# Performance work log

Hardware: AMD Instinct MI355X
Metric: run time of the kernel (lower is better)

## Reference

```python
import jax, jax.numpy as jnp
import numpy as np

N_NODES = 100000
N_EDGES = 1600000
F_IN = 64
HIDDEN = 64
N_CLASSES = 2


def setup_inputs() -> dict:
    key = jax.random.key(0)
    k1, k2, k3, k4, k5, k6 = jax.random.split(key, 6)
    x = jax.random.normal(k1, (N_NODES, F_IN), dtype=jnp.float32)
    edge_index = jax.random.randint(k2, (2, N_EDGES), 0, N_NODES, dtype=jnp.int64)
    # Glorot-ish init for GCNConv linear weights, zero bias (PyG default)
    W1 = jax.random.normal(k3, (F_IN, HIDDEN), dtype=jnp.float32) * (1.0 / np.sqrt(F_IN))
    b1 = jnp.zeros((HIDDEN,), dtype=jnp.float32)
    W2 = jax.random.normal(k4, (HIDDEN, N_CLASSES), dtype=jnp.float32) * (1.0 / np.sqrt(HIDDEN))
    b2 = jnp.zeros((N_CLASSES,), dtype=jnp.float32)
    return {"x": x, "edge_index": edge_index, "W1": W1, "b1": b1, "W2": W2, "b2": b2}


def _gcn_norm(edge_index, num_nodes):
    # Add self-loops, then symmetric normalization D^-1/2 (A+I) D^-1/2
    loops = jnp.arange(num_nodes, dtype=edge_index.dtype)
    row = jnp.concatenate([edge_index[0], loops])  # [E+N] targets
    col = jnp.concatenate([edge_index[1], loops])  # [E+N] sources
    deg = jax.ops.segment_sum(jnp.ones(row.shape[0], jnp.float32), row, num_segments=num_nodes)
    dinv = jnp.where(deg > 0, jax.lax.rsqrt(deg), 0.0)
    norm = dinv[row] * dinv[col]  # [E+N]
    return row, col, norm


def _gcn_conv(x, W, b, row, col, norm, num_nodes):
    h = x @ W                                   # [N, out]
    msg = h[col] * norm[:, None]                # gather + scale, [E+N, out]
    agg = jax.ops.segment_sum(msg, row, num_segments=num_nodes)  # scatter-add
    return agg + b


def reference(x, edge_index, W1, b1, W2, b2):
    n = x.shape[0]
    row, col, norm = _gcn_norm(edge_index, n)
    h = jax.nn.relu(_gcn_conv(x, W1, b1, row, col, norm, n))
    # dropout p=0.5 is identity in eval mode
    logits = _gcn_conv(h, W2, b2, row, col, norm, n)
    return jax.nn.softmax(logits, axis=1)
```

## Files before the change

### kernel.cpp

```cpp
#include <hip/hip_runtime.h>
#include <hip/hip_fp16.h>


typedef _Float16 f16x8 __attribute__((ext_vector_type(8)));
typedef float f32x4 __attribute__((ext_vector_type(4)));

#define CAPSH 12
#define CAP (1 << CAPSH)
#define NBK 784

__global__ __launch_bounds__(256) void k_bin(const int* __restrict__ row,
                                             const int* __restrict__ col,
                                             int* __restrict__ relcur,
                                             unsigned* __restrict__ pairbuf,
                                             __half* __restrict__ hp,
                                             int E, int nb, int N) {
    __shared__ unsigned items[4096];
    __shared__ unsigned short bktid[4096];
    __shared__ int cnt[NBK];
    __shared__ int start0[NBK];
    __shared__ int cursor[NBK];
    __shared__ int gbase[NBK];

    int tid = threadIdx.x;
    int base = blockIdx.x * 4096;
    int m = E - base; if (m > 4096) m = 4096;

    for (int t = tid; t < nb; t += 256) cnt[t] = 0;
    __syncthreads();
    for (int i = tid; i < m; i += 256) atomicAdd(&cnt[row[base + i] >> 7], 1);
    __syncthreads();
    if (tid < 64) {
        int lane = tid, running = 0;
        for (int ch = 0; ch < 13; ++ch) {
            int idx = ch * 64 + lane;
            int v = (idx < nb) ? cnt[idx] : 0;
            int s = v;
#pragma unroll
            for (int off = 1; off < 64; off <<= 1) {
                int t = __shfl_up(s, off, 64);
                if (lane >= off) s += t;
            }
            if (idx < nb) { start0[idx] = running + s - v; cursor[idx] = running + s - v; }
            running += __shfl(s, 63, 64);
        }
    }
    __syncthreads();
    for (int i = tid; i < m; i += 256) {
        int r = row[base + i];
        int c = col[base + i];
        int b = r >> 7;
        int pos = atomicAdd(&cursor[b], 1);
        items[pos] = ((unsigned)(r & 127) << 24) | (unsigned)c;
        bktid[pos] = (unsigned short)b;
    }
    __syncthreads();
    for (int t = tid; t < nb; t += 256) {
        int cv = cnt[t];
        if (cv > 0) gbase[t] = (t << CAPSH) + atomicAdd(&relcur[t], cv);
    }
    __syncthreads();
    for (int i = tid; i < m; i += 256) {
        int b = bktid[i];
        pairbuf[gbase[b] + (i - start0[b])] = items[i];
    }
    if (blockIdx.x == 0 && tid < 32) ((int*)(hp + (size_t)N * 64))[tid] = 0;
}

__global__ __launch_bounds__(256, 4) void k_sortgemm(const unsigned* __restrict__ pairbuf,
                                                     const int* __restrict__ relcur,
                                                     const float* __restrict__ x,
                                                     const float* __restrict__ W1,
                                                     int* __restrict__ scol,
                                                     int* __restrict__ offsets,
                                                     int* __restrict__ deg,
                                                     float* __restrict__ dinv,
                                                     __half* __restrict__ hp,
                                                     int N, int nb) {
    __shared__ int cnt[256];
    __shared__ int tmp[256];
    __shared__ int cur[256];
    __shared__ float sdinv[128];
    int b = blockIdx.x;
    int tid = threadIdx.x;
    int lane = tid & 63, q = lane >> 4, mm = lane & 15;
    f16x8 bf[4][2];
#pragma unroll
    for (int nt = 0; nt < 4; ++nt)
#pragma unroll
        for (int kk = 0; kk < 2; ++kk)
#pragma unroll
            for (int j = 0; j < 8; ++j)
                bf[nt][kk][j] = (_Float16)W1[(kk * 32 + q * 8 + j) * 64 + nt * 16 + mm];

    int lo = b << CAPSH;
    int hi = lo + relcur[b];
    cnt[tid] = 0;
    __syncthreads();
    for (int i = lo + tid; i < hi; i += 256)
        atomicAdd(&cnt[pairbuf[i] >> 24], 1);
    __syncthreads();
    int cv = cnt[tid];
    tmp[tid] = cv;
    __syncthreads();
    for (int d = 1; d < 256; d <<= 1) {
        int t = (tid >= d) ? tmp[tid - d] : 0;
        __syncthreads();
        if (tid >= d) tmp[tid] += t;
        __syncthreads();
    }
    int excl = tmp[tid] - cv;
    int n0 = b << 7;
    if (tid < 128) {
        int n = n0 + tid;
        float dv = rsqrtf((float)(cv + 1));
        if (n < N) { offsets[n] = lo + excl; deg[n] = cv; dinv[n] = dv; }
        sdinv[tid] = dv;
    }
    cur[tid] = lo + excl;
    if (b == 0 && tid == 0) {
        offsets[N] = 0; deg[N] = 0;
        scol[nb << CAPSH] = N;
    }
    __syncthreads();
    for (int i = lo + tid; i < hi; i += 256) {
        unsigned it = pairbuf[i];
        int pos = atomicAdd(&cur[it >> 24], 1);
        scol[pos] = (int)(it & 0xFFFFFFu);
    }
    __syncthreads();
    int nn = N - n0; if (nn > 128) nn = 128;
    for (int t = (tid >> 6); t < (nn >> 4); t += 4) {
        const float* xrow = x + (size_t)(n0 + t * 16 + mm) * 64;
        float4 u0 = *(const float4*)(xrow + q * 8);
        float4 u1 = *(const float4*)(xrow + q * 8 + 4);
        float4 u2 = *(const float4*)(xrow + 32 + q * 8);
        float4 u3 = *(const float4*)(xrow + 32 + q * 8 + 4);
        f16x8 a0, a1;
        a0[0] = (_Float16)u0.x; a0[1] = (_Float16)u0.y; a0[2] = (_Float16)u0.z; a0[3] = (_Float16)u0.w;
        a0[4] = (_Float16)u1.x; a0[5] = (_Float16)u1.y; a0[6] = (_Float16)u1.z; a0[7] = (_Float16)u1.w;
        a1[0] = (_Float16)u2.x; a1[1] = (_Float16)u2.y; a1[2] = (_Float16)u2.z; a1[3] = (_Float16)u2.w;
        a1[4] = (_Float16)u3.x; a1[5] = (_Float16)u3.y; a1[6] = (_Float16)u3.z; a1[7] = (_Float16)u3.w;
        f32x4 ac0 = {0.f, 0.f, 0.f, 0.f}, ac1 = ac0, ac2 = ac0, ac3 = ac0;
        ac0 = __builtin_amdgcn_mfma_f32_16x16x32_f16(a0, bf[0][0], ac0, 0, 0, 0);
        ac1 = __builtin_amdgcn_mfma_f32_16x16x32_f16(a0, bf[1][0], ac1, 0, 0, 0);
        ac2 = __builtin_amdgcn_mfma_f32_16x16x32_f16(a0, bf[2][0], ac2, 0, 0, 0);
        ac3 = __builtin_amdgcn_mfma_f32_16x16x32_f16(a0, bf[3][0], ac3, 0, 0, 0);
        ac0 = __builtin_amdgcn_mfma_f32_16x16x32_f16(a1, bf[0][1], ac0, 0, 0, 0);
        ac1 = __builtin_amdgcn_mfma_f32_16x16x32_f16(a1, bf[1][1], ac1, 0, 0, 0);
        ac2 = __builtin_amdgcn_mfma_f32_16x16x32_f16(a1, bf[2][1], ac2, 0, 0, 0);
        ac3 = __builtin_amdgcn_mfma_f32_16x16x32_f16(a1, bf[3][1], ac3, 0, 0, 0);
#pragma unroll
        for (int reg = 0; reg < 4; ++reg) {
            int rl = t * 16 + q * 4 + reg;
            float dvv = sdinv[rl];
            __half* dst = hp + (size_t)(n0 + rl) * 64 + mm;
            dst[0]  = __float2half(dvv * ac0[reg]);
            dst[16] = __float2half(dvv * ac1[reg]);
            dst[32] = __float2half(dvv * ac2[reg]);
            dst[48] = __float2half(dvv * ac3[reg]);
        }
    }
}

__global__ __launch_bounds__(256, 4) void k_agg1(const __half* __restrict__ hp,
                                                 const int* __restrict__ offsets,
                                                 const int* __restrict__ deg,
                                                 const int* __restrict__ scol,
                                                 const float* __restrict__ dinv,
                                                 const float* __restrict__ b1,
                                                 const float* __restrict__ W2,
                                                 float2* __restrict__ h2p,
                                                 int N, int SENT) {
    int lane = threadIdx.x & 63;
    int slot = lane >> 3;
    int chunk = lane & 7;
    int wid = (int)((blockIdx.x * 256 + threadIdx.x) >> 6);
    int n = wid * 8 + slot;
    int nc = (n < N) ? n : N;
    int start = offsets[nc];
    int dg = deg[nc];
    int maxd = dg;
#pragma unroll
    for (int s = 8; s <= 32; s <<= 1) {
        int o = __shfl_xor(maxd, s, 64);
        maxd = (o > maxd) ? o : maxd;
    }
    const float4* hp4 = (const float4*)hp;
    float4 sr = hp4[(size_t)nc * 8 + chunk];
    __half2 acc0 = ((const __half2*)&sr)[0];
    __half2 acc1 = ((const __half2*)&sr)[1];
    __half2 acc2 = ((const __half2*)&sr)[2];
    __half2 acc3 = ((const __half2*)&sr)[3];
    for (int j0 = 0; j0 < maxd; j0 += 8) {
        int c[8];
#pragma unroll
        for (int u = 0; u < 8; ++u)
            c[u] = scol[(j0 + u < dg) ? (start + j0 + u) : SENT];
        float4 r[8];
#pragma unroll
        for (int u = 0; u < 8; ++u) r[u] = hp4[(size_t)c[u] * 8 + chunk];
#pragma unroll
        for (int u = 0; u < 8; ++u) {
            const __half2* hh = (const __half2*)&r[u];
            acc0 = __hadd2(acc0, hh[0]); acc1 = __hadd2(acc1, hh[1]);
            acc2 = __hadd2(acc2, hh[2]); acc3 = __hadd2(acc3, hh[3]);
        }
    }
    float af[8];
    { float2 f;
      f = __half22float2(acc0); af[0] = f.x; af[1] = f.y;
      f = __half22float2(acc1); af[2] = f.x; af[3] = f.y;
      f = __half22float2(acc2); af[4] = f.x; af[5] = f.y;
      f = __half22float2(acc3); af[6] = f.x; af[7] = f.y; }
    float dn = dinv[(n < N) ? n : (N - 1)];
    float4 b1a = ((const float4*)b1)[chunk * 2];
    float4 b1b = ((const float4*)b1)[chunk * 2 + 1];
    float h1[8];
    h1[0] = fmaxf(fmaf(dn, af[0], b1a.x), 0.f);
    h1[1] = fmaxf(fmaf(dn, af[1], b1a.y), 0.f);
    h1[2] = fmaxf(fmaf(dn, af[2], b1a.z), 0.f);
    h1[3] = fmaxf(fmaf(dn, af[3], b1a.w), 0.f);
    h1[4] = fmaxf(fmaf(dn, af[4], b1b.x), 0.f);
    h1[5] = fmaxf(fmaf(dn, af[5], b1b.y), 0.f);
    h1[6] = fmaxf(fmaf(dn, af[6], b1b.z), 0.f);
    h1[7] = fmaxf(fmaf(dn, af[7], b1b.w), 0.f);
    float p0 = 0.f, p1 = 0.f;
#pragma unroll
    for (int k = 0; k < 4; ++k) {
        float4 w = ((const float4*)W2)[chunk * 4 + k];
        p0 = fmaf(h1[2 * k], w.x, p0); p1 = fmaf(h1[2 * k], w.y, p1);
        p0 = fmaf(h1[2 * k + 1], w.z, p0); p1 = fmaf(h1[2 * k + 1], w.w, p1);
    }
#pragma unroll
    for (int s = 1; s <= 4; s <<= 1) {
        p0 += __shfl_xor(p0, s, 64);
        p1 += __shfl_xor(p1, s, 64);
    }
    if (chunk == 0 && n < N) h2p[n] = make_float2(dn * p0, dn * p1);
}

__global__ __launch_bounds__(256) void k_agg2(const float2* __restrict__ h2p,
                                              const int* __restrict__ offsets,
                                              const int* __restrict__ deg,
                                              const int* __restrict__ scol,
                                              const float* __restrict__ dinv,
                                              const float* __restrict__ b2,
                                              float2* __restrict__ out, int N) {
    int gtid = blockIdx.x * 256 + threadIdx.x;
    int n = gtid >> 4;
    int sub = threadIdx.x & 15;
    if (n >= N) return;
    int start = offsets[n], end = start + deg[n];
    float ax = 0.f, ay = 0.f;
    if (sub == 0) { float2 s = h2p[n]; ax = s.x; ay = s.y; }
    for (int j = start + sub; j < end; j += 16) {
        float2 v = h2p[scol[j]];
        ax += v.x; ay += v.y;
    }
#pragma unroll
    for (int s = 1; s <= 8; s <<= 1) {
        ax += __shfl_xor(ax, s, 64);
        ay += __shfl_xor(ay, s, 64);
    }
    if (sub == 0) {
        float dn = dinv[n];
        float l0 = fmaf(dn, ax, b2[0]), l1 = fmaf(dn, ay, b2[1]);
        float m = fmaxf(l0, l1);
        float e0 = __expf(l0 - m), e1 = __expf(l1 - m);
        float inv = 1.0f / (e0 + e1);
        out[n] = make_float2(e0 * inv, e1 * inv);
    }
}

extern "C" void kernel_launch(void* const* d_in, const int* in_sizes, int n_in,
                              void* d_out, int out_size, void* d_ws, size_t ws_size,
                              hipStream_t stream) {
    const float* x  = (const float*)d_in[0];
    const int*   ei = (const int*)d_in[1];
    const float* W1 = (const float*)d_in[2];
    const float* b1 = (const float*)d_in[3];
    const float* W2 = (const float*)d_in[4];
    const float* b2 = (const float*)d_in[5];
    float2* out = (float2*)d_out;

    const int N = in_sizes[0] / 64;
    const int E = in_sizes[1] / 2;
    const int nb = (N + 127) >> 7;
    const int SENT = nb << CAPSH;
    const int* row = ei;
    const int* col = ei + E;

    char* p = (char*)d_ws;
    auto alloc = [&](size_t bytes) -> void* {
        void* r = (void*)p;
        p += (bytes + 255) & ~(size_t)255;
        return r;
    };
    int*   relcur  = (int*)alloc((size_t)nb * 4);
    int*   offsets = (int*)alloc((size_t)(N + 1) * 4);
    int*   deg     = (int*)alloc((size_t)(N + 1) * 4);
    float* dinv    = (float*)alloc((size_t)N * 4);
    unsigned* pairbuf = (unsigned*)alloc((size_t)nb * CAP * 4);
    int*   scol    = (int*)alloc(((size_t)nb * CAP + 1) * 4);
    __half* hp     = (__half*)alloc((size_t)(N + 1) * 64 * 2);
    float2* h2p    = (float2*)alloc((size_t)N * 8);

    const int nTile = (E + 4095) / 4096;

    hipMemsetAsync(relcur, 0, (size_t)nb * 4, stream);
    k_bin<<<nTile, 256, 0, stream>>>(row, col, relcur, pairbuf, hp, E, nb, N);
    k_sortgemm<<<nb, 256, 0, stream>>>(pairbuf, relcur, x, W1, scol, offsets, deg, dinv, hp, N, nb);
    const int nwaves = (N + 7) / 8;
    k_agg1<<<(nwaves + 3) / 4, 256, 0, stream>>>(hp, offsets, deg, scol, dinv, b1, W2, h2p, N, SENT);
    k_agg2<<<(N * 16 + 255) / 256, 256, 0, stream>>>(h2p, offsets, deg, scol, dinv, b2, out, N);
}
```

Baseline: 166.8 us.

## Run X·W1 GEMM alongside edge binning and defer dinv scaling to sort kernel

The dense X·W1 MFMA GEMM moves out of the per-bucket sort kernel into extra blocks of the binning kernel, so it runs at the same time as edge binning. It writes an fp32 intermediate that the sort kernel later scales by dinv and converts to fp16. The Hillis-Steele shared-memory scan with many barriers is replaced by a wave-level shuffle scan over the 128 row slots. The cost is an extra fp32 round trip of N×64 values (about 25 MB of writes plus reads) and a larger workspace.

```diff
diff --git a/kernel.cpp b/kernel.cpp
--- a/kernel.cpp
+++ b/kernel.cpp
@@ -9,12 +9,15 @@
 #define CAP (1 << CAPSH)
 #define NBK 784
 
-__global__ __launch_bounds__(256) void k_bin(const int* __restrict__ row,
-                                             const int* __restrict__ col,
-                                             int* __restrict__ relcur,
-                                             unsigned* __restrict__ pairbuf,
-                                             __half* __restrict__ hp,
-                                             int E, int nb, int N) {
+__global__ __launch_bounds__(256, 4) void k_binfused(const int* __restrict__ row,
+                                                     const int* __restrict__ col,
+                                                     int* __restrict__ relcur,
+                                                     unsigned* __restrict__ pairbuf,
+                                                     __half* __restrict__ hp,
+                                                     const float* __restrict__ x,
+                                                     const float* __restrict__ W1,
+                                                     float* __restrict__ hf32,
+                                                     int E, int nb, int N, int nTileB) {
     __shared__ unsigned items[4096];
     __shared__ unsigned short bktid[4096];
     __shared__ int cnt[NBK];
@@ -23,76 +26,112 @@
     __shared__ int gbase[NBK];
 
     int tid = threadIdx.x;
-    int base = blockIdx.x * 4096;
-    int m = E - base; if (m > 4096) m = 4096;
-
-    for (int t = tid; t < nb; t += 256) cnt[t] = 0;
-    __syncthreads();
-    for (int i = tid; i < m; i += 256) atomicAdd(&cnt[row[base + i] >> 7], 1);
-    __syncthreads();
-    if (tid < 64) {
-        int lane = tid, running = 0;
-        for (int ch = 0; ch < 13; ++ch) {
-            int idx = ch * 64 + lane;
-            int v = (idx < nb) ? cnt[idx] : 0;
-            int s = v;
-#pragma unroll
-            for (int off = 1; off < 64; off <<= 1) {
-                int t = __shfl_up(s, off, 64);
-                if (lane >= off) s += t;
+
+    if (blockIdx.x < nTileB) {
+        int base = blockIdx.x * 4096;
+        int m = E - base; if (m > 4096) m = 4096;
+
+        for (int t = tid; t < nb; t += 256) cnt[t] = 0;
+        __syncthreads();
+        for (int i = tid; i < m; i += 256) atomicAdd(&cnt[row[base + i] >> 7], 1);
+        __syncthreads();
+        if (tid < 64) {
+            int lane = tid, running = 0;
+            for (int ch = 0; ch < 13; ++ch) {
+                int idx = ch * 64 + lane;
+                int v = (idx < nb) ? cnt[idx] : 0;
+                int s = v;
+#pragma unroll
+                for (int off = 1; off < 64; off <<= 1) {
+                    int t = __shfl_up(s, off, 64);
+                    if (lane >= off) s += t;
+                }
+                if (idx < nb) { start0[idx] = running + s - v; cursor[idx] = running + s - v; }
+                running += __shfl(s, 63, 64);
             }
-            if (idx < nb) { start0[idx] = running + s - v; cursor[idx] = running + s - v; }
-            running += __shfl(s, 63, 64);
-        }
-    }
-    __syncthreads();
-    for (int i = tid; i < m; i += 256) {
-        int r = row[base + i];
-        int c = col[base + i];
-        int b = r >> 7;
-        int pos = atomicAdd(&cursor[b], 1);
-        items[pos] = ((unsigned)(r & 127) << 24) | (unsigned)c;
-        bktid[pos] = (unsigned short)b;
-    }
-    __syncthreads();
-    for (int t = tid; t < nb; t += 256) {
-        int cv = cnt[t];
-        if (cv > 0) gbase[t] = (t << CAPSH) + atomicAdd(&relcur[t], cv);
-    }
-    __syncthreads();
-    for (int i = tid; i < m; i += 256) {
-        int b = bktid[i];
-        pairbuf[gbase[b] + (i - start0[b])] = items[i];
-    }
-    if (blockIdx.x == 0 && tid < 32) ((int*)(hp + (size_t)N * 64))[tid] = 0;
-}
-
-__global__ __launch_bounds__(256, 4) void k_sortgemm(const unsigned* __restrict__ pairbuf,
-                                                     const int* __restrict__ relcur,
-                                                     const float* __restrict__ x,
-                                                     const float* __restrict__ W1,
-                                                     int* __restrict__ scol,
-                                                     int* __restrict__ offsets,
-                                                     int* __restrict__ deg,
-                                                     float* __restrict__ dinv,
-                                                     __half* __restrict__ hp,
-                                                     int N, int nb) {
+        }
+        __syncthreads();
+        for (int i = tid; i < m; i += 256) {
+            int r = row[base + i];
+            int c = col[base + i];
+            int b = r >> 7;
+            int pos = atomicAdd(&cursor[b], 1);
+            items[pos] = ((unsigned)(r & 127) << 24) | (unsigned)c;
+            bktid[pos] = (unsigned short)b;
+        }
+        __syncthreads();
+        for (int t = tid; t < nb; t += 256) {
+            int cv = cnt[t];
+            if (cv > 0) gbase[t] = (t << CAPSH) + atomicAdd(&relcur[t], cv);
+        }
+        __syncthreads();
+        for (int i = tid; i < m; i += 256) {
+            int b = bktid[i];
+            pairbuf[gbase[b] + (i - start0[b])] = items[i];
+        }
+        if (blockIdx.x == 0 && tid < 32) ((int*)(hp + (size_t)N * 64))[tid] = 0;
+    } else {
+        int g = blockIdx.x - nTileB;
+        int n0 = g << 8;
+        int lane = tid & 63, q = lane >> 4, mm = lane & 15;
+        f16x8 bf[4][2];
+#pragma unroll
+        for (int nt = 0; nt < 4; ++nt)
+#pragma unroll
+            for (int kk = 0; kk < 2; ++kk)
+#pragma unroll
+                for (int j = 0; j < 8; ++j)
+                    bf[nt][kk][j] = (_Float16)W1[(kk * 32 + q * 8 + j) * 64 + nt * 16 + mm];
+
+        int nn = N - n0; if (nn > 256) nn = 256;
+        for (int t = (tid >> 6); t < (nn >> 4); t += 4) {
+            const float* xrow = x + (size_t)(n0 + t * 16 + mm) * 64;
+            float4 u0 = *(const float4*)(xrow + q * 8);
+            float4 u1 = *(const float4*)(xrow + q * 8 + 4);
+            float4 u2 = *(const float4*)(xrow + 32 + q * 8);
+            float4 u3 = *(const float4*)(xrow + 32 + q * 8 + 4);
+            f16x8 a0, a1;
+            a0[0] = (_Float16)u0.x; a0[1] = (_Float16)u0.y; a0[2] = (_Float16)u0.z; a0[3] = (_Float16)u0.w;
+            a0[4] = (_Float16)u1.x; a0[5] = (_Float16)u1.y; a0[6] = (_Float16)u1.z; a0[7] = (_Float16)u1.w;
+            a1[0] = (_Float16)u2.x; a1[1] = (_Float16)u2.y; a1[2] = (_Float16)u2.z; a1[3] = (_Float16)u2.w;
+            a1[4] = (_Float16)u3.x; a1[5] = (_Float16)u3.y; a1[6] = (_Float16)u3.z; a1[7] = (_Float16)u3.w;
+            f32x4 ac0 = {0.f, 0.f, 0.f, 0.f}, ac1 = ac0, ac2 = ac0, ac3 = ac0;
+            ac0 = __builtin_amdgcn_mfma_f32_16x16x32_f16(a0, bf[0][0], ac0, 0, 0, 0);
+            ac1 = __builtin_amdgcn_mfma_f32_16x16x32_f16(a0, bf[1][0], ac1, 0, 0, 0);
+            ac2 = __builtin_amdgcn_mfma_f32_16x16x32_f16(a0, bf[2][0], ac2, 0, 0, 0);
+            ac3 = __builtin_amdgcn_mfma_f32_16x16x32_f16(a0, bf[3][0], ac3, 0, 0, 0);
+            ac0 = __builtin_amdgcn_mfma_f32_16x16x32_f16(a1, bf[0][1], ac0, 0, 0, 0);
+            ac1 = __builtin_amdgcn_mfma_f32_16x16x32_f16(a1, bf[1][1], ac1, 0, 0, 0);
+            ac2 = __builtin_amdgcn_mfma_f32_16x16x32_f16(a1, bf[2][1], ac2, 0, 0, 0);
+            ac3 = __builtin_amdgcn_mfma_f32_16x16x32_f16(a1, bf[3][1], ac3, 0, 0, 0);
+#pragma unroll
+            for (int reg = 0; reg < 4; ++reg) {
+                int rl = t * 16 + q * 4 + reg;
+                float* dst = hf32 + (size_t)(n0 + rl) * 64 + mm;
+                dst[0]  = ac0[reg];
+                dst[16] = ac1[reg];
+                dst[32] = ac2[reg];
+                dst[48] = ac3[reg];
+            }
+        }
+    }
+}
+
+__global__ __launch_bounds__(256, 4) void k_sortscale(const unsigned* __restrict__ pairbuf,
+                                                      const int* __restrict__ relcur,
+                                                      const float* __restrict__ hf32,
+                                                      int* __restrict__ scol,
+                                                      int* __restrict__ offsets,
+                                                      int* __restrict__ deg,
+                                                      float* __restrict__ dinv,
+                                                      __half* __restrict__ hp,
+                                                      int N, int nb) {
     __shared__ int cnt[256];
-    __shared__ int tmp[256];
-    __shared__ int cur[256];
+    __shared__ int spre[128];
+    __shared__ int cur[128];
     __shared__ float sdinv[128];
     int b = blockIdx.x;
     int tid = threadIdx.x;
-    int lane = tid & 63, q = lane >> 4, mm = lane & 15;
-    f16x8 bf[4][2];
-#pragma unroll
-    for (int nt = 0; nt < 4; ++nt)
-#pragma unroll
-        for (int kk = 0; kk < 2; ++kk)
-#pragma unroll
-            for (int j = 0; j < 8; ++j)
-                bf[nt][kk][j] = (_Float16)W1[(kk * 32 + q * 8 + j) * 64 + nt * 16 + mm];
-
     int lo = b << CAPSH;
     int hi = lo + relcur[b];
     cnt[tid] = 0;
@@ -100,24 +139,33 @@
     for (int i = lo + tid; i < hi; i += 256)
         atomicAdd(&cnt[pairbuf[i] >> 24], 1);
     __syncthreads();
-    int cv = cnt[tid];
-    tmp[tid] = cv;
+    if (tid < 64) {
+        int lane = tid, running = 0;
+#pragma unroll
+        for (int ch = 0; ch < 2; ++ch) {
+            int idx = ch * 64 + lane;
+            int v = cnt[idx];
+            int s = v;
+#pragma unroll
+            for (int off = 1; off < 64; off <<= 1) {
+                int t = __shfl_up(s, off, 64);
+                if (lane >= off) s += t;
+            }
+            spre[idx] = running + s - v;
+            running += __shfl(s, 63, 64);
+        }
+    }
     __syncthreads();
-    for (int d = 1; d < 256; d <<= 1) {
-        int t = (tid >= d) ? tmp[tid - d] : 0;
-        __syncthreads();
-        if (tid >= d) tmp[tid] += t;
-        __syncthreads();
-    }
-    int excl = tmp[tid] - cv;
     int n0 = b << 7;
     if (tid < 128) {
+        int cv = cnt[tid];
+        int excl = spre[tid];
         int n = n0 + tid;
         float dv = rsqrtf((float)(cv + 1));
         if (n < N) { offsets[n] = lo + excl; deg[n] = cv; dinv[n] = dv; }
         sdinv[tid] = dv;
-    }
-    cur[tid] = lo + excl;
+        cur[tid] = lo + excl;
+    }
     if (b == 0 && tid == 0) {
         offsets[N] = 0; deg[N] = 0;
         scol[nb << CAPSH] = N;
@@ -128,37 +176,22 @@
         int pos = atomicAdd(&cur[it >> 24], 1);
         scol[pos] = (int)(it & 0xFFFFFFu);
     }
-    __syncthreads();
-    int nn = N - n0; if (nn > 128) nn = 128;
-    for (int t = (tid >> 6); t < (nn >> 4); t += 4) {
-        const float* xrow = x + (size_t)(n0 + t * 16 + mm) * 64;
-        float4 u0 = *(const float4*)(xrow + q * 8);
-        float4 u1 = *(const float4*)(xrow + q * 8 + 4);
-        float4 u2 = *(const float4*)(xrow + 32 + q * 8);
-        float4 u3 = *(const float4*)(xrow + 32 + q * 8 + 4);
-        f16x8 a0, a1;
-        a0[0] = (_Float16)u0.x; a0[1] = (_Float16)u0.y; a0[2] = (_Float16)u0.z; a0[3] = (_Float16)u0.w;
-        a0[4] = (_Float16)u1.x; a0[5] = (_Float16)u1.y; a0[6] = (_Float16)u1.z; a0[7] = (_Float16)u1.w;
-        a1[0] = (_Float16)u2.x; a1[1] = (_Float16)u2.y; a1[2] = (_Float16)u2.z; a1[3] = (_Float16)u2.w;
-        a1[4] = (_Float16)u3.x; a1[5] = (_Float16)u3.y; a1[6] = (_Float16)u3.z; a1[7] = (_Float16)u3.w;
-        f32x4 ac0 = {0.f, 0.f, 0.f, 0.f}, ac1 = ac0, ac2 = ac0, ac3 = ac0;
-        ac0 = __builtin_amdgcn_mfma_f32_16x16x32_f16(a0, bf[0][0], ac0, 0, 0, 0);
-        ac1 = __builtin_amdgcn_mfma_f32_16x16x32_f16(a0, bf[1][0], ac1, 0, 0, 0);
-        ac2 = __builtin_amdgcn_mfma_f32_16x16x32_f16(a0, bf[2][0], ac2, 0, 0, 0);
-        ac3 = __builtin_amdgcn_mfma_f32_16x16x32_f16(a0, bf[3][0], ac3, 0, 0, 0);
-        ac0 = __builtin_amdgcn_mfma_f32_16x16x32_f16(a1, bf[0][1], ac0, 0, 0, 0);
-        ac1 = __builtin_amdgcn_mfma_f32_16x16x32_f16(a1, bf[1][1], ac1, 0, 0, 0);
-        ac2 = __builtin_amdgcn_mfma_f32_16x16x32_f16(a1, bf[2][1], ac2, 0, 0, 0);
-        ac3 = __builtin_amdgcn_mfma_f32_16x16x32_f16(a1, bf[3][1], ac3, 0, 0, 0);
-#pragma unroll
-        for (int reg = 0; reg < 4; ++reg) {
-            int rl = t * 16 + q * 4 + reg;
-            float dvv = sdinv[rl];
-            __half* dst = hp + (size_t)(n0 + rl) * 64 + mm;
-            dst[0]  = __float2half(dvv * ac0[reg]);
-            dst[16] = __float2half(dvv * ac1[reg]);
-            dst[32] = __float2half(dvv * ac2[reg]);
-            dst[48] = __float2half(dvv * ac3[reg]);
+    int rowi = tid >> 1, half = tid & 1;
+    int n = n0 + rowi;
+    if (n < N) {
+        float dv = sdinv[rowi];
+        const float4* src = (const float4*)(hf32 + (size_t)n * 64 + half * 32);
+        f16x8* dst = (f16x8*)(hp + (size_t)n * 64 + half * 32);
+#pragma unroll
+        for (int k = 0; k < 4; ++k) {
+            float4 u0 = src[2 * k];
+            float4 u1 = src[2 * k + 1];
+            f16x8 o;
+            o[0] = (_Float16)(dv * u0.x); o[1] = (_Float16)(dv * u0.y);
+            o[2] = (_Float16)(dv * u0.z); o[3] = (_Float16)(dv * u0.w);
+            o[4] = (_Float16)(dv * u1.x); o[5] = (_Float16)(dv * u1.y);
+            o[6] = (_Float16)(dv * u1.z); o[7] = (_Float16)(dv * u1.w);
+            dst[k] = o;
         }
     }
 }
@@ -305,12 +338,15 @@
     int*   scol    = (int*)alloc(((size_t)nb * CAP + 1) * 4);
     __half* hp     = (__half*)alloc((size_t)(N + 1) * 64 * 2);
     float2* h2p    = (float2*)alloc((size_t)N * 8);
-
-    const int nTile = (E + 4095) / 4096;
+    float* hf32    = (float*)alloc((size_t)N * 64 * 4);
+
+    const int nTileB = (E + 4095) / 4096;
+    const int nGemm  = (N + 255) >> 8;
 
     hipMemsetAsync(relcur, 0, (size_t)nb * 4, stream);
-    k_bin<<<nTile, 256, 0, stream>>>(row, col, relcur, pairbuf, hp, E, nb, N);
-    k_sortgemm<<<nb, 256, 0, stream>>>(pairbuf, relcur, x, W1, scol, offsets, deg, dinv, hp, N, nb);
+    k_binfused<<<nTileB + nGemm, 256, 0, stream>>>(row, col, relcur, pairbuf, hp,
+                                                   x, W1, hf32, E, nb, N, nTileB);
+    k_sortscale<<<nb, 256, 0, stream>>>(pairbuf, relcur, hf32, scol, offsets, deg, dinv, hp, N, nb);
     const int nwaves = (N + 7) / 8;
     k_agg1<<<(nwaves + 3) / 4, 256, 0, stream>>>(hp, offsets, deg, scol, dinv, b1, W2, h2p, N, SENT);
     k_agg2<<<(N * 16 + 255) / 256, 256, 0, stream>>>(h2p, offsets, deg, scol, dinv, b2, out, N);
```

Result: no change. 169.7 us (+1.7%).
